# Kernel optimization log

Measured on AMD Instinct MI355X. Metric: run time of the kernel, lower is better.

The kernel has to match this reference:

```python
import jax, jax.numpy as jnp
import numpy as np

N_NODES = 100000
N_EDGES = 600000
IN_CH = 128
HID = 64
N_REL = 8


def setup_inputs() -> dict:
    key = jax.random.key(0)
    ks = jax.random.split(key, 9)
    x = jax.random.normal(ks[0], (N_NODES, IN_CH), dtype=jnp.float32)
    edge_index = jax.random.randint(ks[1], (2, N_EDGES), 0, N_NODES)
    edge_type = jax.random.randint(ks[2], (N_EDGES,), 0, N_REL)
    s_in = 1.0 / np.sqrt(IN_CH)   # torch Linear init bound
    s_h = 1.0 / np.sqrt(HID)
    W_rel = jax.random.uniform(ks[3], (N_REL, HID, IN_CH), minval=-s_in, maxval=s_in, dtype=jnp.float32)
    b_rel = jax.random.uniform(ks[4], (N_REL, HID), minval=-s_in, maxval=s_in, dtype=jnp.float32)
    W_self = jax.random.uniform(ks[5], (HID, IN_CH), minval=-s_in, maxval=s_in, dtype=jnp.float32)
    b_self = jax.random.uniform(ks[6], (HID,), minval=-s_in, maxval=s_in, dtype=jnp.float32)
    W_out = jax.random.uniform(ks[7], (1, HID), minval=-s_h, maxval=s_h, dtype=jnp.float32)
    b_out = jax.random.uniform(ks[8], (1,), minval=-s_h, maxval=s_h, dtype=jnp.float32)
    return {"x": x, "edge_index": edge_index, "edge_type": edge_type,
            "W_rel": W_rel, "b_rel": b_rel, "W_self": W_self, "b_self": b_self,
            "W_out": W_out, "b_out": b_out}


def reference(x, edge_index, edge_type, W_rel, b_rel, W_self, b_self, W_out, b_out):
    row, col = edge_index[0], edge_index[1]
    R, H, _ = W_rel.shape
    N = x.shape[0]
    # Project every node under every relation once ([R, N, H]) instead of the
    # per-relation masked gather->GEMM loop: same math (sum over edges of
    # W_{edge_type} x_{src} + b_{edge_type} scattered into dst).
    xp = jnp.einsum('ni,rhi->rnh', x, W_rel)                     # [R, N, H]
    msg = xp.reshape(R * N, H)[edge_type * N + row] + b_rel[edge_type]  # [E, H]
    agg = jax.ops.segment_sum(msg, col, num_segments=N)          # scatter-add into dst
    out = jax.nn.relu(agg + x @ W_self.T + b_self)               # [N, H]
    return (out @ W_out.T + b_out)[:, 0]                          # [N]
```

## Files before the change

### kernel.cpp

```cpp
#include <hip/hip_runtime.h>
#include <hip/hip_bf16.h>

#define IN_CH    128
#define HID      64
#define N_REL    8
#define KSTEP    36
#define SROW2    580
#define SLOT_CAP 32
#define NBKT     784
#define BKT_CAP  1024

using bf16x8 = __attribute__((ext_vector_type(8))) short;
using f32x4  = __attribute__((ext_vector_type(4))) float;

__device__ __forceinline__ short f2bf(float f) {
    unsigned int u = __float_as_uint(f);
    u += 0x7fffu + ((u >> 16) & 1u);
    return (short)(u >> 16);
}

__device__ __forceinline__ void conv_unit(
    const float* __restrict__ x, unsigned short* __restrict__ xb, int i)
{
    const float* p = x + (size_t)i * 8;
    float4 a = *(const float4*)p;
    float4 c = *(const float4*)(p + 4);
    bf16x8 o;
    o[0]=f2bf(a.x); o[1]=f2bf(a.y); o[2]=f2bf(a.z); o[3]=f2bf(a.w);
    o[4]=f2bf(c.x); o[5]=f2bf(c.y); o[6]=f2bf(c.z); o[7]=f2bf(c.w);
    *(bf16x8*)(xb + (size_t)i * 8) = o;
}

__global__ __launch_bounds__(1024) void k1_kernel(
    const int* __restrict__ edge_index, const int* __restrict__ edge_type,
    unsigned int* __restrict__ gcount, uint2* __restrict__ gbuf, int E, int nbB,
    const float* __restrict__ x, unsigned short* __restrict__ xb, int total8,
    int nbC1,
    const float* __restrict__ W_rel, const float* __restrict__ W_self,
    unsigned short* __restrict__ wpk)
{
    const int b = blockIdx.x, tid = threadIdx.x;
    if (b < nbB) {
        __shared__ unsigned int hist[NBKT];
        for (int i = tid; i < NBKT; i += 1024) hist[i] = 0u;
        __syncthreads();

        const int e0 = (b * 1024 + tid) * 8;
        unsigned int pay[8]; unsigned int dstv[8]; unsigned int rnk[8]; int bkt[8];
        const bool full = (e0 + 8 <= E);
        if (full) {
            int4 s0 = *(const int4*)(edge_index + e0);
            int4 s1 = *(const int4*)(edge_index + e0 + 4);
            int4 d0 = *(const int4*)(edge_index + E + e0);
            int4 d1 = *(const int4*)(edge_index + E + e0 + 4);
            int4 t0 = *(const int4*)(edge_type + e0);
            int4 t1 = *(const int4*)(edge_type + e0 + 4);
            const int* sp0 = &s0.x; const int* sp1 = &s1.x;
            const int* dp0 = &d0.x; const int* dp1 = &d1.x;
            const int* tp0 = &t0.x; const int* tp1 = &t1.x;
            #pragma unroll
            for (int j = 0; j < 4; ++j) {
                pay[j]     = ((unsigned int)sp0[j] << 8) | ((unsigned int)tp0[j] << 28);
                dstv[j]    = (unsigned int)dp0[j];
                pay[j + 4] = ((unsigned int)sp1[j] << 8) | ((unsigned int)tp1[j] << 28);
                dstv[j + 4]= (unsigned int)dp1[j];
            }
            #pragma unroll
            for (int j = 0; j < 8; ++j) {
                bkt[j] = (int)(dstv[j] >> 7);
                rnk[j] = atomicAdd(&hist[bkt[j]], 1u);
            }
        }
        __syncthreads();
        for (int bb = tid; bb < NBKT; bb += 1024) {
            unsigned int c = hist[bb];
            if (c) hist[bb] = atomicAdd(&gcount[bb], c);
        }
        __syncthreads();
        if (full) {
            #pragma unroll
            for (int j = 0; j < 8; ++j) {
                unsigned int p = hist[bkt[j]] + rnk[j];
                if (p < BKT_CAP) {
                    uint2 v; v.x = pay[j]; v.y = dstv[j];
                    gbuf[(size_t)bkt[j] * BKT_CAP + p] = v;
                }
            }
        }
    } else if (b < nbB + nbC1) {
        int i = (b - nbB) * 1024 + tid;
        if (i < total8) conv_unit(x, xb, i);
    } else {
        int gid = (b - nbB - nbC1) * 1024 + tid;
        if (gid >= 9216) return;
        int s2   = gid >> 8;
        int t    = (gid >> 6) & 3;
        int lane = gid & 63;
        int h    = t * 16 + (lane & 15);
        int kb   = s2 * 32 + (lane >> 4) * 8;
        bf16x8 o;
        #pragma unroll
        for (int j = 0; j < 8; ++j) {
            int k = kb + j;
            float v = (k < 1024)
                ? W_rel[(size_t)(k >> 7) * HID * IN_CH + (size_t)h * IN_CH + (k & 127)]
                : W_self[(size_t)h * IN_CH + (k - 1024)];
            o[j] = f2bf(v);
        }
        *(bf16x8*)(wpk + (size_t)gid * 8) = o;
    }
}

__global__ __launch_bounds__(256) void k2_kernel(
    const unsigned int* __restrict__ gcount, const uint2* __restrict__ gbuf,
    int* __restrict__ cnt, unsigned int* __restrict__ slots, int N, int nbS,
    const float* __restrict__ x, unsigned short* __restrict__ xb, int total8,
    int convOff)
{
    const int b = blockIdx.x, tid = threadIdx.x;
    if (b < nbS) {
        __shared__ unsigned int hist[128];
        if (tid < 128) hist[tid] = 0u;
        __syncthreads();
        unsigned int bc = gcount[b]; if (bc > BKT_CAP) bc = BKT_CAP;
        for (unsigned int i = tid; i < bc; i += 256) {
            uint2 v = gbuf[(size_t)b * BKT_CAP + i];
            unsigned int d = v.y;
            unsigned int r = atomicAdd(&hist[d & 127], 1u);
            if (r < SLOT_CAP) slots[(size_t)d * SLOT_CAP + r] = v.x;
        }
        __syncthreads();
        if (tid < 128) {
            int d = b * 128 + tid;
            if (d < N) cnt[d] = (int)hist[tid];
        }
    } else {
        int i = convOff + (b - nbS) * 256 + tid;
        if (i < total8) conv_unit(x, xb, i);
    }
}

__global__ __launch_bounds__(1024, 8) void rgcn_fused_kernel(
    const unsigned int* __restrict__ xbu,
    const unsigned short* __restrict__ wpk,
    const int* __restrict__ cnt,
    const unsigned int* __restrict__ slots,
    const float* __restrict__ b_rel,
    const float* __restrict__ b_self,
    const float* __restrict__ W_out,
    const float* __restrict__ b_out,
    float* __restrict__ out,
    int N)
{
    __shared__ unsigned int Sb[16 * SROW2];
    __shared__ int cntS[16 * 8];
    const int tid  = threadIdx.x;
    const int wave = tid >> 6;
    const int lane = tid & 63;
    const int l16  = lane & 15;
    const int quad = lane >> 4;
    const int nb   = blockIdx.x * 16;
    const int gnode = nb + wave;

    const unsigned int selfv = xbu[(size_t)gnode * 64 + lane];
    const int rawdeg = cnt[gnode];
    unsigned int ev = 0u;
    if (lane < SLOT_CAP)
        ev = slots[(size_t)gnode * SLOT_CAP + lane];
    const int deg = (rawdeg > SLOT_CAP) ? SLOT_CAP : rawdeg;

    const int myr = (lane < deg) ? (int)(ev >> 28) : 8;
    const unsigned long long below =
        (lane == 63) ? 0x7FFFFFFFFFFFFFFFull : ((1ull << lane) - 1ull);
    int rank = 0, off = 0;
    int cw[8];
    #pragma unroll
    for (int r = 0; r < 8; ++r) {
        unsigned long long m = __ballot(myr == r);
        int c = __popcll(m);
        cw[r] = c;
        if (lane == 0) cntS[wave * 8 + r] = c;
        if (myr == r) rank = off + (int)__popcll(m & below);
        off += c;
    }
    {
        unsigned long long minv = __ballot(myr == 8);
        if (myr == 8) rank = off + (int)__popcll(minv & below);
    }
    const int evs = __builtin_amdgcn_ds_permute(rank << 2, (int)ev);

    {
        const char* xbase = (const char*)xbu + (lane << 2);
        unsigned int* Srow = &Sb[wave * SROW2];
        float s0 = 0.f, s1 = 0.f;
        int cur_r = -1;
        for (int e0 = 0; e0 < deg; e0 += 8) {
            int bn = deg - e0; if (bn > 8) bn = 8;
            unsigned int sv[8], uu[8];
            #pragma unroll
            for (int i = 0; i < 8; ++i) {
                if (i < bn) {
                    sv[i] = (unsigned int)__builtin_amdgcn_readlane(evs, e0 + i);
                    uu[i] = *(const unsigned int*)(xbase + (sv[i] & 0x0FFFFFFFu));
                }
            }
            #pragma unroll
            for (int i = 0; i < 8; ++i) {
                if (i >= bn) break;
                const int r = (int)(sv[i] >> 28);
                if (r != cur_r) {
                    if (cur_r >= 0) {
                        unsigned int p =
                            ((unsigned int)(unsigned short)f2bf(s1) << 16)
                          | (unsigned int)(unsigned short)f2bf(s0);
                        Srow[cur_r * 64 + lane] = p;
                    }
                    cur_r = r; s0 = 0.f; s1 = 0.f;
                }
                s0 += __uint_as_float(uu[i] << 16);
                s1 += __uint_as_float(uu[i] & 0xffff0000u);
            }
        }
        if (cur_r >= 0) {
            unsigned int p = ((unsigned int)(unsigned short)f2bf(s1) << 16)
                           | (unsigned int)(unsigned short)f2bf(s0);
            Srow[cur_r * 64 + lane] = p;
        }
        #pragma unroll
        for (int r = 0; r < 8; ++r)
            if (cw[r] == 0) Srow[r * 64 + lane] = 0u;
        Srow[512 + lane] = selfv;
    }
    __syncthreads();

    f32x4 acc[4] = {{0.f,0.f,0.f,0.f},{0.f,0.f,0.f,0.f},
                    {0.f,0.f,0.f,0.f},{0.f,0.f,0.f,0.f}};
    if (wave < 8) {
        const bf16x8* wv = (const bf16x8*)wpk;
        const int s0w = (wave < 4) ? wave * 5 : 20 + (wave - 4) * 4;
        const int ns  = (wave < 4) ? 5 : 4;
        for (int q = 0; q < ns; ++q) {
            const int s2 = s0w + q;
            bf16x8 a[4];
            #pragma unroll
            for (int t = 0; t < 4; ++t)
                a[t] = wv[(size_t)((s2 * 4 + t) * 64) + lane];
            bf16x8 bfrag = *(const bf16x8*)&Sb[l16 * SROW2 + s2 * 16 + quad * 4];
            #pragma unroll
            for (int t = 0; t < 4; ++t)
                acc[t] = __builtin_amdgcn_mfma_f32_16x16x32_bf16(
                    a[t], bfrag, acc[t], 0, 0, 0);
        }
    }
    __syncthreads();

    float* Pf = (float*)Sb;
    if (wave < 8) {
        #pragma unroll
        for (int t = 0; t < 4; ++t)
            *(f32x4*)&Pf[wave * 1100 + l16 * 68 + t * 16 + quad * 4] = acc[t];
    }
    __syncthreads();

    if (tid < 256) {
        const int node = tid & 15, hg = tid >> 4;
        f32x4 v = {0.f, 0.f, 0.f, 0.f};
        #pragma unroll
        for (int w2 = 0; w2 < 8; ++w2)
            v += *(const f32x4*)&Pf[w2 * 1100 + node * 68 + hg * 4];
        float4 bs = *(const float4*)(b_self + hg * 4);
        float4 wo = *(const float4*)(W_out + hg * 4);
        float cb[4] = {0.f, 0.f, 0.f, 0.f};
        #pragma unroll
        for (int r = 0; r < 8; ++r) {
            float cf = (float)cntS[node * 8 + r];
            if (cf != 0.f) {
                float4 br = *(const float4*)(b_rel + r * HID + hg * 4);
                cb[0] += cf * br.x; cb[1] += cf * br.y;
                cb[2] += cf * br.z; cb[3] += cf * br.w;
            }
        }
        float part = 0.f;
        #pragma unroll
        for (int j = 0; j < 4; ++j) {
            float u = v[j] + (&bs.x)[j] + cb[j];
            u = fmaxf(u, 0.f);
            part += u * (&wo.x)[j];
        }
        Pf[8800 + hg * 16 + node] = part;
    }
    __syncthreads();
    if (tid < 16) {
        float sum = 0.f;
        #pragma unroll
        for (int hg = 0; hg < 16; ++hg) sum += Pf[8800 + hg * 16 + tid];
        out[nb + tid] = sum + b_out[0];
    }
}

extern "C" void kernel_launch(void* const* d_in, const int* in_sizes, int n_in,
                              void* d_out, int out_size, void* d_ws, size_t ws_size,
                              hipStream_t stream)
{
    const float* x          = (const float*)d_in[0];
    const int*   edge_index = (const int*)  d_in[1];
    const int*   edge_type  = (const int*)  d_in[2];
    const float* W_rel      = (const float*)d_in[3];
    const float* b_rel      = (const float*)d_in[4];
    const float* W_self     = (const float*)d_in[5];
    const float* b_self     = (const float*)d_in[6];
    const float* W_out      = (const float*)d_in[7];
    const float* b_out      = (const float*)d_in[8];
    float* out = (float*)d_out;

    const int N = in_sizes[0] / IN_CH;
    const int E = in_sizes[2];

    char* w = (char*)d_ws;
    unsigned short* xb  = (unsigned short*)w;  w += (size_t)N * IN_CH * 2;
    unsigned short* wpk = (unsigned short*)w;  w += (size_t)KSTEP * 4 * 64 * 8 * 2;
    int* cnt            = (int*)w;             w += (size_t)N * 4;
    unsigned int* slots = (unsigned int*)w;    w += (size_t)N * SLOT_CAP * 4;
    unsigned int* gcount= (unsigned int*)w;    w += (size_t)NBKT * 4;
    uint2* gbuf         = (uint2*)w;           w += (size_t)NBKT * BKT_CAP * 8;

    const int total8 = N * IN_CH / 8;
    const int nbB    = (E + 8191) / 8192;
    const int nbC1   = ((total8 * 2) / 3 + 1023) / 1024;
    int convDone     = nbC1 * 1024;
    if (convDone > total8) convDone = total8;
    const int nbC2   = (total8 - convDone + 255) / 256;
    const int nbW    = (9216 + 1023) / 1024;

    hipMemsetAsync(gcount, 0, (size_t)NBKT * 4, stream);

    k1_kernel<<<nbB + nbC1 + nbW, 1024, 0, stream>>>(
        edge_index, edge_type, gcount, gbuf, E, nbB,
        x, xb, total8, nbC1, W_rel, W_self, wpk);

    k2_kernel<<<NBKT + nbC2, 256, 0, stream>>>(
        gcount, gbuf, cnt, slots, N, NBKT,
        x, xb, total8, nbC1 * 1024);

    rgcn_fused_kernel<<<N / 16, 1024, 0, stream>>>(
        (const unsigned int*)xb, wpk, cnt, slots,
        b_rel, b_self, W_out, b_out, out, N);
}
```

Before: 216.2 us.

## Project nodes per relation first, then gather projected bf16 rows

Reorders the computation. All nodes are first projected under all 8 relations plus the self weights with MFMA into a bf16 [N,576] buffer z. A lightweight per-node kernel then gathers 64-wide projected rows per edge, replacing the earlier aggregate-then-GEMM fused kernel. The memset is folded into a weight-prep kernel. This drops the per-block LDS staging and the 1152-wide GEMM, but writes and reads a roughly 115MB intermediate, trading compute for memory traffic. It also adds an extra bf16 rounding of messages before they are summed.

After: 228.8 us. +5.8%, slower.

```diff
diff --git a/kernel.cpp b/kernel.cpp
--- a/kernel.cpp
+++ b/kernel.cpp
@@ -4,11 +4,11 @@
 #define IN_CH    128
 #define HID      64
 #define N_REL    8
-#define KSTEP    36
-#define SROW2    580
+#define ZCH      576
 #define SLOT_CAP 32
 #define NBKT     784
 #define BKT_CAP  1024
+#define ZBLK     128
 
 using bf16x8 = __attribute__((ext_vector_type(8))) short;
 using f32x4  = __attribute__((ext_vector_type(4))) float;
@@ -19,32 +19,46 @@
     return (short)(u >> 16);
 }
 
-__device__ __forceinline__ void conv_unit(
-    const float* __restrict__ x, unsigned short* __restrict__ xb, int i)
-{
-    const float* p = x + (size_t)i * 8;
-    float4 a = *(const float4*)p;
-    float4 c = *(const float4*)(p + 4);
-    bf16x8 o;
-    o[0]=f2bf(a.x); o[1]=f2bf(a.y); o[2]=f2bf(a.z); o[3]=f2bf(a.w);
-    o[4]=f2bf(c.x); o[5]=f2bf(c.y); o[6]=f2bf(c.z); o[7]=f2bf(c.w);
-    *(bf16x8*)(xb + (size_t)i * 8) = o;
+__global__ __launch_bounds__(1024) void prep0_kernel(
+    const float* __restrict__ W_rel, const float* __restrict__ W_self,
+    unsigned short* __restrict__ wpk2, unsigned int* __restrict__ gcount)
+{
+    const int b = blockIdx.x, tid = threadIdx.x;
+    if (b < 9) {
+        int gid  = b * 1024 + tid;
+        int kt   = gid / 2304;
+        int rem  = gid - kt * 2304;
+        int mt   = rem >> 6;
+        int lane = rem & 63;
+        int ch   = mt * 16 + (lane & 15);
+        int k0   = kt * 32 + ((lane >> 4) << 3);
+        bf16x8 o;
+        #pragma unroll
+        for (int j = 0; j < 8; ++j) {
+            int k = k0 + j;
+            float v = (ch < 512)
+                ? W_rel[(size_t)(ch >> 6) * (HID * IN_CH) + (size_t)(ch & 63) * IN_CH + k]
+                : W_self[(size_t)(ch - 512) * IN_CH + k];
+            o[j] = f2bf(v);
+        }
+        *(bf16x8*)(wpk2 + (size_t)gid * 8) = o;
+    } else {
+        if (tid < NBKT) gcount[tid] = 0u;
+    }
 }
 
 __global__ __launch_bounds__(1024) void k1_kernel(
     const int* __restrict__ edge_index, const int* __restrict__ edge_type,
     unsigned int* __restrict__ gcount, uint2* __restrict__ gbuf, int E, int nbB,
-    const float* __restrict__ x, unsigned short* __restrict__ xb, int total8,
-    int nbC1,
-    const float* __restrict__ W_rel, const float* __restrict__ W_self,
-    unsigned short* __restrict__ wpk)
-{
+    const float* __restrict__ x, const unsigned short* __restrict__ wpk2,
+    unsigned short* __restrict__ z, int N)
+{
+    __shared__ unsigned int hist[NBKT];
+    __shared__ short xs[ZBLK * 136];
     const int b = blockIdx.x, tid = threadIdx.x;
     if (b < nbB) {
-        __shared__ unsigned int hist[NBKT];
         for (int i = tid; i < NBKT; i += 1024) hist[i] = 0u;
         __syncthreads();
-
         const int e0 = (b * 1024 + tid) * 8;
         unsigned int pay[8]; unsigned int dstv[8]; unsigned int rnk[8]; int bkt[8];
         const bool full = (e0 + 8 <= E);
@@ -60,9 +74,11 @@
             const int* tp0 = &t0.x; const int* tp1 = &t1.x;
             #pragma unroll
             for (int j = 0; j < 4; ++j) {
-                pay[j]     = ((unsigned int)sp0[j] << 8) | ((unsigned int)tp0[j] << 28);
+                pay[j]     = (unsigned int)sp0[j] * 1152u
+                           + ((unsigned int)tp0[j] << 7) + ((unsigned int)tp0[j] << 28);
                 dstv[j]    = (unsigned int)dp0[j];
-                pay[j + 4] = ((unsigned int)sp1[j] << 8) | ((unsigned int)tp1[j] << 28);
+                pay[j + 4] = (unsigned int)sp1[j] * 1152u
+                           + ((unsigned int)tp1[j] << 7) + ((unsigned int)tp1[j] << 28);
                 dstv[j + 4]= (unsigned int)dp1[j];
             }
             #pragma unroll
@@ -87,215 +103,127 @@
                 }
             }
         }
-    } else if (b < nbB + nbC1) {
-        int i = (b - nbB) * 1024 + tid;
-        if (i < total8) conv_unit(x, xb, i);
     } else {
-        int gid = (b - nbB - nbC1) * 1024 + tid;
-        if (gid >= 9216) return;
-        int s2   = gid >> 8;
-        int t    = (gid >> 6) & 3;
-        int lane = gid & 63;
-        int h    = t * 16 + (lane & 15);
-        int kb   = s2 * 32 + (lane >> 4) * 8;
-        bf16x8 o;
-        #pragma unroll
-        for (int j = 0; j < 8; ++j) {
-            int k = kb + j;
-            float v = (k < 1024)
-                ? W_rel[(size_t)(k >> 7) * HID * IN_CH + (size_t)h * IN_CH + (k & 127)]
-                : W_self[(size_t)h * IN_CH + (k - 1024)];
-            o[j] = f2bf(v);
-        }
-        *(bf16x8*)(wpk + (size_t)gid * 8) = o;
+        const int nodebase = (b - nbB) * ZBLK;
+        {
+            int node = tid >> 3;
+            int ch0  = (tid & 7) * 16;
+            int ng   = nodebase + node;
+            if (ng < N) {
+                const float* p = x + (size_t)ng * IN_CH + ch0;
+                float4 a0 = *(const float4*)p;
+                float4 a1 = *(const float4*)(p + 4);
+                float4 a2 = *(const float4*)(p + 8);
+                float4 a3 = *(const float4*)(p + 12);
+                bf16x8 o0, o1;
+                o0[0]=f2bf(a0.x); o0[1]=f2bf(a0.y); o0[2]=f2bf(a0.z); o0[3]=f2bf(a0.w);
+                o0[4]=f2bf(a1.x); o0[5]=f2bf(a1.y); o0[6]=f2bf(a1.z); o0[7]=f2bf(a1.w);
+                o1[0]=f2bf(a2.x); o1[1]=f2bf(a2.y); o1[2]=f2bf(a2.z); o1[3]=f2bf(a2.w);
+                o1[4]=f2bf(a3.x); o1[5]=f2bf(a3.y); o1[6]=f2bf(a3.z); o1[7]=f2bf(a3.w);
+                *(bf16x8*)(xs + node * 136 + ch0)     = o0;
+                *(bf16x8*)(xs + node * 136 + ch0 + 8) = o1;
+            }
+        }
+        __syncthreads();
+        const int wave = tid >> 6, lane = tid & 63;
+        const int nt   = wave >> 1;
+        const int mt0  = (wave & 1) * 18;
+        const short* abase = xs + (nt * 16 + (lane & 15)) * 136 + ((lane >> 4) << 3);
+        const bf16x8* wv = (const bf16x8*)wpk2;
+        const int nbase = nodebase + nt * 16 + ((lane >> 4) << 2);
+        for (int mti = 0; mti < 18; ++mti) {
+            const int mt = mt0 + mti;
+            f32x4 acc = {0.f, 0.f, 0.f, 0.f};
+            #pragma unroll
+            for (int kt = 0; kt < 4; ++kt) {
+                bf16x8 a  = *(const bf16x8*)(abase + kt * 32);
+                bf16x8 bb = wv[(size_t)((kt * 36 + mt) * 64) + lane];
+                acc = __builtin_amdgcn_mfma_f32_16x16x32_bf16(a, bb, acc, 0, 0, 0);
+            }
+            const int ch = mt * 16 + (lane & 15);
+            #pragma unroll
+            for (int j = 0; j < 4; ++j) {
+                int n = nbase + j;
+                if (n < N)
+                    z[(size_t)n * ZCH + ch] = (unsigned short)f2bf(acc[j]);
+            }
+        }
     }
 }
 
 __global__ __launch_bounds__(256) void k2_kernel(
     const unsigned int* __restrict__ gcount, const uint2* __restrict__ gbuf,
-    int* __restrict__ cnt, unsigned int* __restrict__ slots, int N, int nbS,
-    const float* __restrict__ x, unsigned short* __restrict__ xb, int total8,
-    int convOff)
-{
+    int* __restrict__ cnt, unsigned int* __restrict__ slots, int N)
+{
+    __shared__ unsigned int hist[128];
     const int b = blockIdx.x, tid = threadIdx.x;
-    if (b < nbS) {
-        __shared__ unsigned int hist[128];
-        if (tid < 128) hist[tid] = 0u;
-        __syncthreads();
-        unsigned int bc = gcount[b]; if (bc > BKT_CAP) bc = BKT_CAP;
-        for (unsigned int i = tid; i < bc; i += 256) {
-            uint2 v = gbuf[(size_t)b * BKT_CAP + i];
-            unsigned int d = v.y;
-            unsigned int r = atomicAdd(&hist[d & 127], 1u);
-            if (r < SLOT_CAP) slots[(size_t)d * SLOT_CAP + r] = v.x;
-        }
-        __syncthreads();
-        if (tid < 128) {
-            int d = b * 128 + tid;
-            if (d < N) cnt[d] = (int)hist[tid];
-        }
-    } else {
-        int i = convOff + (b - nbS) * 256 + tid;
-        if (i < total8) conv_unit(x, xb, i);
-    }
-}
-
-__global__ __launch_bounds__(1024, 8) void rgcn_fused_kernel(
-    const unsigned int* __restrict__ xbu,
-    const unsigned short* __restrict__ wpk,
-    const int* __restrict__ cnt,
+    if (tid < 128) hist[tid] = 0u;
+    __syncthreads();
+    unsigned int bc = gcount[b]; if (bc > BKT_CAP) bc = BKT_CAP;
+    for (unsigned int i = tid; i < bc; i += 256) {
+        uint2 v = gbuf[(size_t)b * BKT_CAP + i];
+        unsigned int d = v.y;
+        unsigned int r = atomicAdd(&hist[d & 127], 1u);
+        if (r < SLOT_CAP) slots[(size_t)d * SLOT_CAP + r] = v.x;
+    }
+    __syncthreads();
+    if (tid < 128) {
+        int d = b * 128 + tid;
+        if (d < N) cnt[d] = (int)hist[tid];
+    }
+}
+
+__global__ __launch_bounds__(256) void agg_kernel(
+    const unsigned short* __restrict__ z, const int* __restrict__ cnt,
     const unsigned int* __restrict__ slots,
-    const float* __restrict__ b_rel,
-    const float* __restrict__ b_self,
-    const float* __restrict__ W_out,
-    const float* __restrict__ b_out,
-    float* __restrict__ out,
-    int N)
-{
-    __shared__ unsigned int Sb[16 * SROW2];
-    __shared__ int cntS[16 * 8];
+    const float* __restrict__ b_rel, const float* __restrict__ b_self,
+    const float* __restrict__ W_out, const float* __restrict__ b_out,
+    float* __restrict__ out, int N)
+{
     const int tid  = threadIdx.x;
-    const int wave = tid >> 6;
+    const int g    = blockIdx.x * 4 + (tid >> 6);
     const int lane = tid & 63;
-    const int l16  = lane & 15;
-    const int quad = lane >> 4;
-    const int nb   = blockIdx.x * 16;
-    const int gnode = nb + wave;
-
-    const unsigned int selfv = xbu[(size_t)gnode * 64 + lane];
-    const int rawdeg = cnt[gnode];
+
+    const int rawdeg = cnt[g];
     unsigned int ev = 0u;
-    if (lane < SLOT_CAP)
-        ev = slots[(size_t)gnode * SLOT_CAP + lane];
+    if (lane < SLOT_CAP) ev = slots[(size_t)g * SLOT_CAP + lane];
+    const float selfv =
+        __uint_as_float((unsigned int)z[(size_t)g * ZCH + 512 + lane] << 16);
+
     const int deg = (rawdeg > SLOT_CAP) ? SLOT_CAP : rawdeg;
-
     const int myr = (lane < deg) ? (int)(ev >> 28) : 8;
-    const unsigned long long below =
-        (lane == 63) ? 0x7FFFFFFFFFFFFFFFull : ((1ull << lane) - 1ull);
-    int rank = 0, off = 0;
-    int cw[8];
+    int cr[8];
     #pragma unroll
-    for (int r = 0; r < 8; ++r) {
-        unsigned long long m = __ballot(myr == r);
-        int c = __popcll(m);
-        cw[r] = c;
-        if (lane == 0) cntS[wave * 8 + r] = c;
-        if (myr == r) rank = off + (int)__popcll(m & below);
-        off += c;
-    }
-    {
-        unsigned long long minv = __ballot(myr == 8);
-        if (myr == 8) rank = off + (int)__popcll(minv & below);
-    }
-    const int evs = __builtin_amdgcn_ds_permute(rank << 2, (int)ev);
-
-    {
-        const char* xbase = (const char*)xbu + (lane << 2);
-        unsigned int* Srow = &Sb[wave * SROW2];
-        float s0 = 0.f, s1 = 0.f;
-        int cur_r = -1;
-        for (int e0 = 0; e0 < deg; e0 += 8) {
-            int bn = deg - e0; if (bn > 8) bn = 8;
-            unsigned int sv[8], uu[8];
-            #pragma unroll
-            for (int i = 0; i < 8; ++i) {
-                if (i < bn) {
-                    sv[i] = (unsigned int)__builtin_amdgcn_readlane(evs, e0 + i);
-                    uu[i] = *(const unsigned int*)(xbase + (sv[i] & 0x0FFFFFFFu));
-                }
-            }
-            #pragma unroll
-            for (int i = 0; i < 8; ++i) {
-                if (i >= bn) break;
-                const int r = (int)(sv[i] >> 28);
-                if (r != cur_r) {
-                    if (cur_r >= 0) {
-                        unsigned int p =
-                            ((unsigned int)(unsigned short)f2bf(s1) << 16)
-                          | (unsigned int)(unsigned short)f2bf(s0);
-                        Srow[cur_r * 64 + lane] = p;
-                    }
-                    cur_r = r; s0 = 0.f; s1 = 0.f;
-                }
-                s0 += __uint_as_float(uu[i] << 16);
-                s1 += __uint_as_float(uu[i] & 0xffff0000u);
-            }
-        }
-        if (cur_r >= 0) {
-            unsigned int p = ((unsigned int)(unsigned short)f2bf(s1) << 16)
-                           | (unsigned int)(unsigned short)f2bf(s0);
-            Srow[cur_r * 64 + lane] = p;
-        }
+    for (int r = 0; r < 8; ++r) cr[r] = (int)__popcll(__ballot(myr == r));
+
+    const char* zb = (const char*)z;
+    float agg = 0.f;
+    for (int e0 = 0; e0 < deg; e0 += 8) {
+        int bn = deg - e0; if (bn > 8) bn = 8;
+        unsigned int sv[8]; unsigned short gv[8];
         #pragma unroll
-        for (int r = 0; r < 8; ++r)
-            if (cw[r] == 0) Srow[r * 64 + lane] = 0u;
-        Srow[512 + lane] = selfv;
-    }
-    __syncthreads();
-
-    f32x4 acc[4] = {{0.f,0.f,0.f,0.f},{0.f,0.f,0.f,0.f},
-                    {0.f,0.f,0.f,0.f},{0.f,0.f,0.f,0.f}};
-    if (wave < 8) {
-        const bf16x8* wv = (const bf16x8*)wpk;
-        const int s0w = (wave < 4) ? wave * 5 : 20 + (wave - 4) * 4;
-        const int ns  = (wave < 4) ? 5 : 4;
-        for (int q = 0; q < ns; ++q) {
-            const int s2 = s0w + q;
-            bf16x8 a[4];
-            #pragma unroll
-            for (int t = 0; t < 4; ++t)
-                a[t] = wv[(size_t)((s2 * 4 + t) * 64) + lane];
-            bf16x8 bfrag = *(const bf16x8*)&Sb[l16 * SROW2 + s2 * 16 + quad * 4];
-            #pragma unroll
-            for (int t = 0; t < 4; ++t)
-                acc[t] = __builtin_amdgcn_mfma_f32_16x16x32_bf16(
-                    a[t], bfrag, acc[t], 0, 0, 0);
-        }
-    }
-    __syncthreads();
-
-    float* Pf = (float*)Sb;
-    if (wave < 8) {
+        for (int i = 0; i < 8; ++i) {
+            if (i < bn) {
+                sv[i] = (unsigned int)__builtin_amdgcn_readlane((int)ev, e0 + i);
+                gv[i] = *(const unsigned short*)(zb + (sv[i] & 0x0FFFFFFFu) + (lane << 1));
+            }
+        }
         #pragma unroll
-        for (int t = 0; t < 4; ++t)
-            *(f32x4*)&Pf[wave * 1100 + l16 * 68 + t * 16 + quad * 4] = acc[t];
-    }
-    __syncthreads();
-
-    if (tid < 256) {
-        const int node = tid & 15, hg = tid >> 4;
-        f32x4 v = {0.f, 0.f, 0.f, 0.f};
-        #pragma unroll
-        for (int w2 = 0; w2 < 8; ++w2)
-            v += *(const f32x4*)&Pf[w2 * 1100 + node * 68 + hg * 4];
-        float4 bs = *(const float4*)(b_self + hg * 4);
-        float4 wo = *(const float4*)(W_out + hg * 4);
-        float cb[4] = {0.f, 0.f, 0.f, 0.f};
-        #pragma unroll
-        for (int r = 0; r < 8; ++r) {
-            float cf = (float)cntS[node * 8 + r];
-            if (cf != 0.f) {
-                float4 br = *(const float4*)(b_rel + r * HID + hg * 4);
-                cb[0] += cf * br.x; cb[1] += cf * br.y;
-                cb[2] += cf * br.z; cb[3] += cf * br.w;
-            }
-        }
-        float part = 0.f;
-        #pragma unroll
-        for (int j = 0; j < 4; ++j) {
-            float u = v[j] + (&bs.x)[j] + cb[j];
-            u = fmaxf(u, 0.f);
-            part += u * (&wo.x)[j];
-        }
-        Pf[8800 + hg * 16 + node] = part;
-    }
-    __syncthreads();
-    if (tid < 16) {
-        float sum = 0.f;
-        #pragma unroll
-        for (int hg = 0; hg < 16; ++hg) sum += Pf[8800 + hg * 16 + tid];
-        out[nb + tid] = sum + b_out[0];
-    }
+        for (int i = 0; i < 8; ++i) {
+            if (i >= bn) break;
+            agg += __uint_as_float((unsigned int)gv[i] << 16);
+        }
+    }
+
+    float h = agg + selfv + b_self[lane];
+    #pragma unroll
+    for (int r = 0; r < 8; ++r)
+        h += (float)cr[r] * b_rel[r * HID + lane];
+    h = fmaxf(h, 0.f) * W_out[lane];
+    #pragma unroll
+    for (int m = 32; m >= 1; m >>= 1)
+        h += __shfl_xor(h, m, 64);
+    if (lane == 0) out[g] = h + b_out[0];
 }
 
 extern "C" void kernel_launch(void* const* d_in, const int* in_sizes, int n_in,
@@ -317,32 +245,23 @@
     const int E = in_sizes[2];
 
     char* w = (char*)d_ws;
-    unsigned short* xb  = (unsigned short*)w;  w += (size_t)N * IN_CH * 2;
-    unsigned short* wpk = (unsigned short*)w;  w += (size_t)KSTEP * 4 * 64 * 8 * 2;
-    int* cnt            = (int*)w;             w += (size_t)N * 4;
-    unsigned int* slots = (unsigned int*)w;    w += (size_t)N * SLOT_CAP * 4;
-    unsigned int* gcount= (unsigned int*)w;    w += (size_t)NBKT * 4;
-    uint2* gbuf         = (uint2*)w;           w += (size_t)NBKT * BKT_CAP * 8;
-
-    const int total8 = N * IN_CH / 8;
-    const int nbB    = (E + 8191) / 8192;
-    const int nbC1   = ((total8 * 2) / 3 + 1023) / 1024;
-    int convDone     = nbC1 * 1024;
-    if (convDone > total8) convDone = total8;
-    const int nbC2   = (total8 - convDone + 255) / 256;
-    const int nbW    = (9216 + 1023) / 1024;
-
-    hipMemsetAsync(gcount, 0, (size_t)NBKT * 4, stream);
-
-    k1_kernel<<<nbB + nbC1 + nbW, 1024, 0, stream>>>(
-        edge_index, edge_type, gcount, gbuf, E, nbB,
-        x, xb, total8, nbC1, W_rel, W_self, wpk);
-
-    k2_kernel<<<NBKT + nbC2, 256, 0, stream>>>(
-        gcount, gbuf, cnt, slots, N, NBKT,
-        x, xb, total8, nbC1 * 1024);
-
-    rgcn_fused_kernel<<<N / 16, 1024, 0, stream>>>(
-        (const unsigned int*)xb, wpk, cnt, slots,
-        b_rel, b_self, W_out, b_out, out, N);
-}
+    unsigned short* wpk2 = (unsigned short*)w; w += 147456;
+    int* cnt             = (int*)w;            w += ((size_t)N * 4 + 255) & ~255ull;
+    unsigned int* slots  = (unsigned int*)w;   w += (size_t)N * SLOT_CAP * 4;
+    unsigned int* gcount = (unsigned int*)w;   w += (NBKT * 4 + 255) & ~255;
+    uint2* gbuf          = (uint2*)w;          w += (size_t)NBKT * BKT_CAP * 8;
+    unsigned short* z    = (unsigned short*)w; w += (size_t)N * ZCH * 2;
+
+    const int nbB     = (E + 8191) / 8192;
+    const int zblocks = (N + ZBLK - 1) / ZBLK;
+
+    prep0_kernel<<<10, 1024, 0, stream>>>(W_rel, W_self, wpk2, gcount);
+
+    k1_kernel<<<nbB + zblocks, 1024, 0, stream>>>(
+        edge_index, edge_type, gcount, gbuf, E, nbB, x, wpk2, z, N);
+
+    k2_kernel<<<NBKT, 256, 0, stream>>>(gcount, gbuf, cnt, slots, N);
+
+    agg_kernel<<<N / 4, 256, 0, stream>>>(
+        z, cnt, slots, b_rel, b_self, W_out, b_out, out, N);
+}
```
